# Kernel tuning notes

Hardware: AMD Instinct MI355X
Metric: run time of the kernel (lower is better)

Reference implementation:

```python
import jax, jax.numpy as jnp
import numpy as np

N_NODES = 100000
N_EDGES = 1600000


def _glorot(key, shape):
    lim = float(np.sqrt(6.0 / (shape[0] + shape[1])))
    return jax.random.uniform(key, shape, jnp.float32, -lim, lim)


def setup_inputs() -> dict:
    key = jax.random.key(0)
    ks = jax.random.split(key, 12)
    x = jax.random.normal(ks[0], (N_NODES, 8), jnp.float32)
    edge_index = jax.random.randint(ks[1], (2, N_EDGES), 0, N_NODES, jnp.int64)
    dims = [(8, 32), (32, 32), (32, 32), (32, 32), (32, 3)]
    params = {}
    for i, (din, dout) in enumerate(dims):
        params[f"W{i+1}"] = _glorot(ks[2 + i], (din, dout))
        params[f"b{i+1}"] = jnp.zeros((dout,), jnp.float32)
    return {"x": x, "edge_index": edge_index, **params}


def _gcn_norm(edge_index, num_nodes):
    # add self-loops, symmetric normalization (PyG GCNConv defaults)
    loops = jnp.arange(num_nodes, dtype=edge_index.dtype)
    row = jnp.concatenate([edge_index[0], loops])
    col = jnp.concatenate([edge_index[1], loops])
    deg = jax.ops.segment_sum(jnp.ones_like(col, jnp.float32), col,
                              num_segments=num_nodes)
    dinv = jnp.where(deg > 0, jax.lax.rsqrt(deg), 0.0)
    norm = dinv[row] * dinv[col]  # [E + N]
    return row, col, norm


def _gcn_conv(h, W, b, row, col, norm, num_nodes):
    h = h @ W                                   # [N, dout]
    msg = h[row] * norm[:, None]                # gather + scale
    out = jax.ops.segment_sum(msg, col, num_segments=num_nodes)
    return out + b


def reference(x, edge_index, W1, b1, W2, b2, W3, b3, W4, b4, W5, b5):
    row, col, norm = _gcn_norm(edge_index, N_NODES)
    lrelu = lambda h: jax.nn.leaky_relu(h, negative_slope=1.0)  # identity, kept faithful
    h = lrelu(_gcn_conv(x, W1, b1, row, col, norm, N_NODES))
    h = lrelu(_gcn_conv(h, W2, b2, row, col, norm, N_NODES))
    h = lrelu(_gcn_conv(h, W3, b3, row, col, norm, N_NODES))
    h = lrelu(_gcn_conv(h, W4, b4, row, col, norm, N_NODES))
    h = lrelu(_gcn_conv(h, W5, b5, row, col, norm, N_NODES))
    return h
```

## Files before the change

kernel.cpp:

```cpp
#include <hip/hip_runtime.h>
#include <hip/hip_bf16.h>

#define NN 100000
#define NE 1600000
#define NB 391
#define EPB 4096
#define NBLK 391
#define CAP 4608



__global__ __launch_bounds__(256) void prep_kernel(
    const unsigned int* __restrict__ ew, int* __restrict__ is64,
    const float* __restrict__ W1, const float* __restrict__ b1,
    const float* __restrict__ W2, const float* __restrict__ b2,
    const float* __restrict__ W3, const float* __restrict__ b3,
    const float* __restrict__ W4, const float* __restrict__ b4,
    const float* __restrict__ W5, const float* __restrict__ b5,
    float* __restrict__ Wt, float* __restrict__ cv,
    int* __restrict__ bcursor) {
    __shared__ int nz;
    __shared__ float w45[32 * 3], w345[32 * 3], w2345[32 * 3];
    int tid = threadIdx.x;
    if (tid == 0) nz = 0;
    __syncthreads();
    if (ew[2 * tid + 1] != 0) atomicAdd(&nz, 1);
    for (int i = tid; i < NB; i += 256) bcursor[i] = i * CAP;
    int i = tid / 3, j = tid - 3 * (tid / 3);
    if (tid < 96) {
        float s = 0.0f;
        for (int k = 0; k < 32; k++) s += W4[i * 32 + k] * W5[k * 3 + j];
        w45[i * 3 + j] = s;
    }
    __syncthreads();
    if (tid < 96) {
        float s = 0.0f;
        for (int k = 0; k < 32; k++) s += W3[i * 32 + k] * w45[k * 3 + j];
        w345[i * 3 + j] = s;
    }
    __syncthreads();
    if (tid < 96) {
        float s = 0.0f;
        for (int k = 0; k < 32; k++) s += W2[i * 32 + k] * w345[k * 3 + j];
        w2345[i * 3 + j] = s;
    }
    __syncthreads();
    if (tid < 32) {
        int ii = tid >> 2, jj = tid & 3;
        float s = 0.0f;
        if (jj < 3)
            for (int k = 0; k < 32; k++) s += W1[ii * 32 + k] * w2345[k * 3 + jj];
        Wt[tid] = s;
    }
    if (tid >= 32 && tid < 52) {
        int kk = (tid - 32) >> 2, jj = (tid - 32) & 3;
        float s = 0.0f;
        if (jj < 3) {
            if (kk == 0) for (int k = 0; k < 32; k++) s += b1[k] * w2345[k * 3 + jj];
            if (kk == 1) for (int k = 0; k < 32; k++) s += b2[k] * w345[k * 3 + jj];
            if (kk == 2) for (int k = 0; k < 32; k++) s += b3[k] * w45[k * 3 + jj];
            if (kk == 3) for (int k = 0; k < 32; k++) s += b4[k] * W5[k * 3 + jj];
            if (kk == 4) s = b5[jj];
        }
        cv[tid - 32] = s;
    }
    if (tid == 0) *is64 = (nz == 0) ? 1 : 0;
}


__global__ __launch_bounds__(512) void bucket_scatter_kernel(const void* __restrict__ ei,
                                                             const int* __restrict__ is64,
                                                             int* __restrict__ bcursor,
                                                             unsigned int* __restrict__ epacked,
                                                             int E) {
    __shared__ int lcount[NB];
    __shared__ int lstart[NB];
    __shared__ int lcur[NB];
    __shared__ int gbase[NB];
    __shared__ int ps[512];
    __shared__ unsigned int slotv[EPB];
    __shared__ unsigned short slotb[EPB];
    int tid = threadIdx.x;
    for (int i = tid; i < NB; i += 512) lcount[i] = 0;
    __syncthreads();
    int f = *is64;
    int base = blockIdx.x * EPB;
    int r[8], c[8];
    if (f == 0) {
        const int* e32 = (const int*)ei;
        const int4* e4 = (const int4*)ei;
#pragma unroll
        for (int k4 = 0; k4 < 2; k4++) {
            int e = base + (k4 * 512 + tid) * 4;
            if (e + 3 < E) {
                int4 v = e4[(base >> 2) + k4 * 512 + tid];
                r[4 * k4 + 0] = v.x; r[4 * k4 + 1] = v.y;
                r[4 * k4 + 2] = v.z; r[4 * k4 + 3] = v.w;
                int4 w = e4[((E + base) >> 2) + k4 * 512 + tid];
                c[4 * k4 + 0] = w.x; c[4 * k4 + 1] = w.y;
                c[4 * k4 + 2] = w.z; c[4 * k4 + 3] = w.w;
            } else {
#pragma unroll
                for (int j = 0; j < 4; j++) {
                    if (e + j < E) {
                        r[4 * k4 + j] = e32[e + j];
                        c[4 * k4 + j] = e32[E + e + j];
                    } else {
                        r[4 * k4 + j] = -1;
                    }
                }
            }
        }
    } else {
        const long long* e64 = (const long long*)ei;
#pragma unroll
        for (int k = 0; k < 8; k++) {
            int e = base + k * 512 + tid;
            if (e < E) {
                r[k] = (int)e64[e];
                c[k] = (int)e64[(long long)E + e];
            } else {
                r[k] = -1;
            }
        }
    }
#pragma unroll
    for (int k = 0; k < 8; k++)
        if (r[k] >= 0) atomicAdd(&lcount[c[k] >> 8], 1);
    __syncthreads();
    int v = (tid < NB) ? lcount[tid] : 0;
    int acc = v;
    ps[tid] = v;
    __syncthreads();
    for (int off = 1; off < 512; off <<= 1) {
        int y = (tid >= off) ? ps[tid - off] : 0;
        __syncthreads();
        acc += y;
        ps[tid] = acc;
        __syncthreads();
    }
    if (tid < NB) {
        int excl = acc - v;
        lstart[tid] = excl;
        lcur[tid] = excl;
    }
    __syncthreads();
#pragma unroll
    for (int k = 0; k < 8; k++) {
        if (r[k] >= 0) {
            int b = c[k] >> 8;
            int pos = atomicAdd(&lcur[b], 1);
            slotv[pos] = ((unsigned)(c[k] & 255) << 24) | (unsigned)r[k];
            slotb[pos] = (unsigned short)b;
        }
    }
    __syncthreads();
    for (int i = tid; i < NB; i += 512) {
        int cnt = lcount[i];
        gbase[i] = cnt ? atomicAdd(&bcursor[i], cnt) : 0;
    }
    __syncthreads();
    int rem = E - base;
    int total = (rem < EPB) ? rem : EPB;
    for (int s2 = tid; s2 < total; s2 += 512) {
        int b = slotb[s2];
        int dst = gbase[b] + (s2 - lstart[b]);
        if (dst < (b + 1) * CAP) epacked[dst] = slotv[s2];
    }
}


__global__ __launch_bounds__(512) void bucket_csr_kernel(const unsigned int* __restrict__ epacked,
                                                         const int* __restrict__ bcursor,
                                                         const float* __restrict__ x,
                                                         const float* __restrict__ Wt,
                                                         int* __restrict__ start,
                                                         int* __restrict__ degi,
                                                         float* __restrict__ dinv,
                                                         int* __restrict__ srow,
                                                         float4* __restrict__ Ta, int N) {
    __shared__ int lcount[256];
    __shared__ int lcur[256];
    __shared__ int ss[256];
    __shared__ float4 Wl[8];
    int b = blockIdx.x;
    int tid = threadIdx.x;
    if (tid < 8) Wl[tid] = ((const float4*)Wt)[tid];
    int s0 = b * CAP;
    int cnt = bcursor[b] - s0;
    if (cnt > CAP) cnt = CAP;
    if (tid < 256) lcount[tid] = 0;
    __syncthreads();
    for (int i = tid; i < cnt; i += 512) {
        unsigned int v = epacked[s0 + i];
        atomicAdd(&lcount[v >> 24], 1);
    }
    __syncthreads();
    int myc = 0, acc = 0;
    if (tid < 256) {
        myc = lcount[tid];
        acc = myc;
        ss[tid] = myc;
    }
    __syncthreads();
    for (int off = 1; off < 256; off <<= 1) {
        int y = 0;
        if (tid < 256 && tid >= off) y = ss[tid - off];
        __syncthreads();
        if (tid < 256) {
            acc += y;
            ss[tid] = acc;
        }
        __syncthreads();
    }
    if (tid < 256) {
        int excl = acc - myc;
        lcur[tid] = excl;
        int col = (b << 8) + tid;
        if (col < N) {
            start[col] = s0 + excl;
            degi[col] = myc;
            float d = 1.0f / sqrtf((float)myc + 1.0f);
            dinv[col] = d;
            const float4* x4 = (const float4*)x + col * 2;
            float4 av = x4[0], bv = x4[1];
            float xs[8] = {av.x, av.y, av.z, av.w, bv.x, bv.y, bv.z, bv.w};
            float4 o = make_float4(0.f, 0.f, 0.f, 0.f);
#pragma unroll
            for (int k = 0; k < 8; k++) {
                float4 w = Wl[k];
                o.x += xs[k] * w.x; o.y += xs[k] * w.y; o.z += xs[k] * w.z;
            }
            o.x *= d; o.y *= d; o.z *= d; o.w = 0.0f;
            Ta[col] = o;
        }
    }
    __syncthreads();
    for (int i = tid; i < cnt; i += 512) {
        unsigned int v = epacked[s0 + i];
        int p = atomicAdd(&lcur[v >> 24], 1);
        srow[s0 + p] = (int)(v & 0xFFFFFFu);
    }
}


template <bool LAST>
__global__ __launch_bounds__(256) void prop_kernel(
    const int* __restrict__ start, const int* __restrict__ degi,
    const int* __restrict__ srow, const float4* __restrict__ tin,
    const float* __restrict__ dinv, const float* __restrict__ cv, int k,
    float4* __restrict__ tout, float* __restrict__ out, int N) {
    int tid = blockIdx.x * 256 + threadIdx.x;
    int c = tid >> 3, q = tid & 7;
    if (c >= N) return;
    int s = start[c];
    int d = degi[c];
    float4 a = (q == 0) ? tin[c] : make_float4(0.f, 0.f, 0.f, 0.f);
    float4 a2 = make_float4(0.f, 0.f, 0.f, 0.f);
    int i = q;
    for (; i + 8 < d; i += 16) {
        int r0 = srow[s + i];
        int r1 = srow[s + i + 8];
        float4 v0 = tin[r0];
        float4 v1 = tin[r1];
        a.x += v0.x; a.y += v0.y; a.z += v0.z;
        a2.x += v1.x; a2.y += v1.y; a2.z += v1.z;
    }
    if (i < d) {
        float4 v = tin[srow[s + i]];
        a.x += v.x; a.y += v.y; a.z += v.z;
    }
    a.x += a2.x; a.y += a2.y; a.z += a2.z;
    a.x += __shfl_xor(a.x, 1); a.y += __shfl_xor(a.y, 1); a.z += __shfl_xor(a.z, 1);
    a.x += __shfl_xor(a.x, 2); a.y += __shfl_xor(a.y, 2); a.z += __shfl_xor(a.z, 2);
    a.x += __shfl_xor(a.x, 4); a.y += __shfl_xor(a.y, 4); a.z += __shfl_xor(a.z, 4);
    if (q == 0) {
        float dd = dinv[c];
        float cx = cv[k * 4 + 0], cy = cv[k * 4 + 1], cz = cv[k * 4 + 2];
        if (LAST) {
            out[c * 3 + 0] = dd * a.x + cx;
            out[c * 3 + 1] = dd * a.y + cy;
            out[c * 3 + 2] = dd * a.z + cz;
        } else {
            float d2 = dd * dd;
            float4 o;
            o.x = d2 * a.x + dd * cx;
            o.y = d2 * a.y + dd * cy;
            o.z = d2 * a.z + dd * cz;
            o.w = 0.0f;
            tout[c] = o;
        }
    }
}


extern "C" void kernel_launch(void* const* d_in, const int* in_sizes, int n_in,
                              void* d_out, int out_size, void* d_ws, size_t ws_size,
                              hipStream_t stream) {
    const float* x  = (const float*)d_in[0];
    const void*  ei = d_in[1];
    const float* W1 = (const float*)d_in[2];  const float* b1 = (const float*)d_in[3];
    const float* W2 = (const float*)d_in[4];  const float* b2 = (const float*)d_in[5];
    const float* W3 = (const float*)d_in[6];  const float* b3 = (const float*)d_in[7];
    const float* W4 = (const float*)d_in[8];  const float* b4 = (const float*)d_in[9];
    const float* W5 = (const float*)d_in[10]; const float* b5 = (const float*)d_in[11];
    float* out = (float*)d_out;

    char* p = (char*)d_ws;
    auto alloc = [&](size_t bytes) {
        char* r = p;
        p += (bytes + 255) & ~(size_t)255;
        return r;
    };
    int*   degi    = (int*)alloc(NN * 4);
    float* dinv    = (float*)alloc(NN * 4);
    int*   start   = (int*)alloc(NN * 4);
    int*   is64    = (int*)alloc(256);
    int*   bcursor = (int*)alloc(NB * 4);
    float* Wt      = (float*)alloc(8 * 4 * 4);
    float* cv      = (float*)alloc(5 * 4 * 4);
    unsigned int* epacked = (unsigned int*)alloc((size_t)NB * CAP * 4);
    int*          srow    = (int*)alloc((size_t)NB * CAP * 4);
    float4*       Ta      = (float4*)alloc((size_t)NN * 16);
    float4*       Tb      = (float4*)alloc((size_t)NN * 16);
    if ((size_t)(p - (char*)d_ws) > ws_size) return;

    int gP = (NN * 8 + 255) / 256;
    prep_kernel<<<1, 256, 0, stream>>>((const unsigned int*)ei, is64,
                                       W1, b1, W2, b2, W3, b3, W4, b4, W5, b5,
                                       Wt, cv, bcursor);
    bucket_scatter_kernel<<<NBLK, 512, 0, stream>>>(ei, is64, bcursor, epacked, NE);
    bucket_csr_kernel<<<NB, 512, 0, stream>>>(epacked, bcursor, x, Wt,
                                              start, degi, dinv, srow, Ta, NN);

    prop_kernel<false><<<gP, 256, 0, stream>>>(start, degi, srow, Ta, dinv, cv, 0, Tb, nullptr, NN);
    prop_kernel<false><<<gP, 256, 0, stream>>>(start, degi, srow, Tb, dinv, cv, 1, Ta, nullptr, NN);
    prop_kernel<false><<<gP, 256, 0, stream>>>(start, degi, srow, Ta, dinv, cv, 2, Tb, nullptr, NN);
    prop_kernel<false><<<gP, 256, 0, stream>>>(start, degi, srow, Tb, dinv, cv, 3, Ta, nullptr, NN);
    prop_kernel<true><<<gP, 256, 0, stream>>>(start, degi, srow, Ta, dinv, cv, 4, nullptr, out, NN);
}
```

Before: 173.0 us.

## Retune bucket scatter grid, use wave-shuffle scans, pack CSR metadata, narrow prop lanes

Splits edges across 512 scatter blocks of 3125 edges, dropping the vectorized int4 loads and the tail checks. Both prefix scans now use wavefront shuffle scans instead of LDS Hillis-Steele loops with many barriers. The CSR kernel stages the sorted rows in LDS so the srow writes are coalesced, and it packs start and degree into one int2 meta array. The prop kernels now use 4 lanes per node instead of 8 and recompute dinv from the degree instead of loading it. The goal is less global traffic, fewer barriers and better occupancy, at the cost of hardcoding NE and less parallelism per high-degree node.

```diff
diff --git a/kernel.cpp b/kernel.cpp
--- a/kernel.cpp
+++ b/kernel.cpp
@@ -4,8 +4,8 @@
 #define NN 100000
 #define NE 1600000
 #define NB 391
-#define EPB 4096
-#define NBLK 391
+#define EPB 3125
+#define NBLK 512
 #define CAP 4608
 
 
@@ -71,13 +71,12 @@
 __global__ __launch_bounds__(512) void bucket_scatter_kernel(const void* __restrict__ ei,
                                                              const int* __restrict__ is64,
                                                              int* __restrict__ bcursor,
-                                                             unsigned int* __restrict__ epacked,
-                                                             int E) {
+                                                             unsigned int* __restrict__ epacked) {
     __shared__ int lcount[NB];
     __shared__ int lstart[NB];
     __shared__ int lcur[NB];
     __shared__ int gbase[NB];
-    __shared__ int ps[512];
+    __shared__ int wsum[8];
     __shared__ unsigned int slotv[EPB];
     __shared__ unsigned short slotb[EPB];
     int tid = threadIdx.x;
@@ -85,68 +84,68 @@
     __syncthreads();
     int f = *is64;
     int base = blockIdx.x * EPB;
-    int r[8], c[8];
+    int r[7], c[7];
+    r[6] = -1;
     if (f == 0) {
         const int* e32 = (const int*)ei;
-        const int4* e4 = (const int4*)ei;
-#pragma unroll
-        for (int k4 = 0; k4 < 2; k4++) {
-            int e = base + (k4 * 512 + tid) * 4;
-            if (e + 3 < E) {
-                int4 v = e4[(base >> 2) + k4 * 512 + tid];
-                r[4 * k4 + 0] = v.x; r[4 * k4 + 1] = v.y;
-                r[4 * k4 + 2] = v.z; r[4 * k4 + 3] = v.w;
-                int4 w = e4[((E + base) >> 2) + k4 * 512 + tid];
-                c[4 * k4 + 0] = w.x; c[4 * k4 + 1] = w.y;
-                c[4 * k4 + 2] = w.z; c[4 * k4 + 3] = w.w;
-            } else {
-#pragma unroll
-                for (int j = 0; j < 4; j++) {
-                    if (e + j < E) {
-                        r[4 * k4 + j] = e32[e + j];
-                        c[4 * k4 + j] = e32[E + e + j];
-                    } else {
-                        r[4 * k4 + j] = -1;
-                    }
-                }
-            }
+#pragma unroll
+        for (int k = 0; k < 6; k++) {
+            int e = base + k * 512 + tid;
+            r[k] = e32[e];
+            c[k] = e32[NE + e];
+        }
+        if (tid < EPB - 6 * 512) {
+            int e = base + 6 * 512 + tid;
+            r[6] = e32[e];
+            c[6] = e32[NE + e];
         }
     } else {
         const long long* e64 = (const long long*)ei;
 #pragma unroll
-        for (int k = 0; k < 8; k++) {
+        for (int k = 0; k < 6; k++) {
             int e = base + k * 512 + tid;
-            if (e < E) {
-                r[k] = (int)e64[e];
-                c[k] = (int)e64[(long long)E + e];
-            } else {
-                r[k] = -1;
-            }
-        }
-    }
-#pragma unroll
-    for (int k = 0; k < 8; k++)
+            r[k] = (int)e64[e];
+            c[k] = (int)e64[(long long)NE + e];
+        }
+        if (tid < EPB - 6 * 512) {
+            int e = base + 6 * 512 + tid;
+            r[6] = (int)e64[e];
+            c[6] = (int)e64[(long long)NE + e];
+        }
+    }
+#pragma unroll
+    for (int k = 0; k < 7; k++)
         if (r[k] >= 0) atomicAdd(&lcount[c[k] >> 8], 1);
     __syncthreads();
+    int lane = tid & 63, w = tid >> 6;
     int v = (tid < NB) ? lcount[tid] : 0;
     int acc = v;
-    ps[tid] = v;
-    __syncthreads();
-    for (int off = 1; off < 512; off <<= 1) {
-        int y = (tid >= off) ? ps[tid - off] : 0;
-        __syncthreads();
-        acc += y;
-        ps[tid] = acc;
-        __syncthreads();
-    }
+#pragma unroll
+    for (int off = 1; off < 64; off <<= 1) {
+        int y = __shfl_up(acc, off);
+        if (lane >= off) acc += y;
+    }
+    if (lane == 63) wsum[w] = acc;
+    __syncthreads();
+    if (tid == 0) {
+        int s = 0;
+#pragma unroll
+        for (int j = 0; j < 8; j++) { int t = wsum[j]; wsum[j] = s; s += t; }
+    }
+    __syncthreads();
+    acc += wsum[w];
     if (tid < NB) {
         int excl = acc - v;
         lstart[tid] = excl;
         lcur[tid] = excl;
     }
-    __syncthreads();
-#pragma unroll
-    for (int k = 0; k < 8; k++) {
+    for (int i = tid; i < NB; i += 512) {
+        int cnt = lcount[i];
+        gbase[i] = cnt ? atomicAdd(&bcursor[i], cnt) : 0;
+    }
+    __syncthreads();
+#pragma unroll
+    for (int k = 0; k < 7; k++) {
         if (r[k] >= 0) {
             int b = c[k] >> 8;
             int pos = atomicAdd(&lcur[b], 1);
@@ -155,14 +154,7 @@
         }
     }
     __syncthreads();
-    for (int i = tid; i < NB; i += 512) {
-        int cnt = lcount[i];
-        gbase[i] = cnt ? atomicAdd(&bcursor[i], cnt) : 0;
-    }
-    __syncthreads();
-    int rem = E - base;
-    int total = (rem < EPB) ? rem : EPB;
-    for (int s2 = tid; s2 < total; s2 += 512) {
+    for (int s2 = tid; s2 < EPB; s2 += 512) {
         int b = slotb[s2];
         int dst = gbase[b] + (s2 - lstart[b]);
         if (dst < (b + 1) * CAP) epacked[dst] = slotv[s2];
@@ -174,15 +166,14 @@
                                                          const int* __restrict__ bcursor,
                                                          const float* __restrict__ x,
                                                          const float* __restrict__ Wt,
-                                                         int* __restrict__ start,
-                                                         int* __restrict__ degi,
-                                                         float* __restrict__ dinv,
+                                                         int2* __restrict__ meta,
                                                          int* __restrict__ srow,
                                                          float4* __restrict__ Ta, int N) {
     __shared__ int lcount[256];
     __shared__ int lcur[256];
-    __shared__ int ss[256];
+    __shared__ int wsum[4];
     __shared__ float4 Wl[8];
+    __shared__ int sbuf[CAP];
     int b = blockIdx.x;
     int tid = threadIdx.x;
     if (tid < 8) Wl[tid] = ((const float4*)Wt)[tid];
@@ -196,40 +187,37 @@
         atomicAdd(&lcount[v >> 24], 1);
     }
     __syncthreads();
-    int myc = 0, acc = 0;
+    int lane = tid & 63, w = tid >> 6;
+    int myc = (tid < 256) ? lcount[tid] : 0;
+    int acc = myc;
+#pragma unroll
+    for (int off = 1; off < 64; off <<= 1) {
+        int y = __shfl_up(acc, off);
+        if (lane >= off) acc += y;
+    }
+    if (lane == 63 && w < 4) wsum[w] = acc;
+    __syncthreads();
+    if (tid == 0) {
+        int s = 0;
+#pragma unroll
+        for (int j = 0; j < 4; j++) { int t = wsum[j]; wsum[j] = s; s += t; }
+    }
+    __syncthreads();
     if (tid < 256) {
-        myc = lcount[tid];
-        acc = myc;
-        ss[tid] = myc;
-    }
-    __syncthreads();
-    for (int off = 1; off < 256; off <<= 1) {
-        int y = 0;
-        if (tid < 256 && tid >= off) y = ss[tid - off];
-        __syncthreads();
-        if (tid < 256) {
-            acc += y;
-            ss[tid] = acc;
-        }
-        __syncthreads();
-    }
-    if (tid < 256) {
-        int excl = acc - myc;
+        int excl = acc - myc + wsum[w];
         lcur[tid] = excl;
         int col = (b << 8) + tid;
         if (col < N) {
-            start[col] = s0 + excl;
-            degi[col] = myc;
+            meta[col] = make_int2(s0 + excl, myc);
             float d = 1.0f / sqrtf((float)myc + 1.0f);
-            dinv[col] = d;
             const float4* x4 = (const float4*)x + col * 2;
             float4 av = x4[0], bv = x4[1];
             float xs[8] = {av.x, av.y, av.z, av.w, bv.x, bv.y, bv.z, bv.w};
             float4 o = make_float4(0.f, 0.f, 0.f, 0.f);
 #pragma unroll
             for (int k = 0; k < 8; k++) {
-                float4 w = Wl[k];
-                o.x += xs[k] * w.x; o.y += xs[k] * w.y; o.z += xs[k] * w.z;
+                float4 ww = Wl[k];
+                o.x += xs[k] * ww.x; o.y += xs[k] * ww.y; o.z += xs[k] * ww.z;
             }
             o.x *= d; o.y *= d; o.z *= d; o.w = 0.0f;
             Ta[col] = o;
@@ -239,28 +227,30 @@
     for (int i = tid; i < cnt; i += 512) {
         unsigned int v = epacked[s0 + i];
         int p = atomicAdd(&lcur[v >> 24], 1);
-        srow[s0 + p] = (int)(v & 0xFFFFFFu);
-    }
+        sbuf[p] = (int)(v & 0xFFFFFFu);
+    }
+    __syncthreads();
+    for (int i = tid; i < cnt; i += 512) srow[s0 + i] = sbuf[i];
 }
 
 
 template <bool LAST>
 __global__ __launch_bounds__(256) void prop_kernel(
-    const int* __restrict__ start, const int* __restrict__ degi,
-    const int* __restrict__ srow, const float4* __restrict__ tin,
-    const float* __restrict__ dinv, const float* __restrict__ cv, int k,
+    const int2* __restrict__ meta, const int* __restrict__ srow,
+    const float4* __restrict__ tin, const float* __restrict__ cv, int k,
     float4* __restrict__ tout, float* __restrict__ out, int N) {
     int tid = blockIdx.x * 256 + threadIdx.x;
-    int c = tid >> 3, q = tid & 7;
+    int c = tid >> 2, q = tid & 3;
     if (c >= N) return;
-    int s = start[c];
-    int d = degi[c];
+    int2 m = meta[c];
+    int s = m.x;
+    int d = m.y;
     float4 a = (q == 0) ? tin[c] : make_float4(0.f, 0.f, 0.f, 0.f);
     float4 a2 = make_float4(0.f, 0.f, 0.f, 0.f);
     int i = q;
-    for (; i + 8 < d; i += 16) {
+    for (; i + 4 < d; i += 8) {
         int r0 = srow[s + i];
-        int r1 = srow[s + i + 8];
+        int r1 = srow[s + i + 4];
         float4 v0 = tin[r0];
         float4 v1 = tin[r1];
         a.x += v0.x; a.y += v0.y; a.z += v0.z;
@@ -273,9 +263,8 @@
     a.x += a2.x; a.y += a2.y; a.z += a2.z;
     a.x += __shfl_xor(a.x, 1); a.y += __shfl_xor(a.y, 1); a.z += __shfl_xor(a.z, 1);
     a.x += __shfl_xor(a.x, 2); a.y += __shfl_xor(a.y, 2); a.z += __shfl_xor(a.z, 2);
-    a.x += __shfl_xor(a.x, 4); a.y += __shfl_xor(a.y, 4); a.z += __shfl_xor(a.z, 4);
     if (q == 0) {
-        float dd = dinv[c];
+        float dd = 1.0f / sqrtf((float)d + 1.0f);
         float cx = cv[k * 4 + 0], cy = cv[k * 4 + 1], cz = cv[k * 4 + 2];
         if (LAST) {
             out[c * 3 + 0] = dd * a.x + cx;
@@ -312,9 +301,7 @@
         p += (bytes + 255) & ~(size_t)255;
         return r;
     };
-    int*   degi    = (int*)alloc(NN * 4);
-    float* dinv    = (float*)alloc(NN * 4);
-    int*   start   = (int*)alloc(NN * 4);
+    int2*  meta    = (int2*)alloc((size_t)NN * 8);
     int*   is64    = (int*)alloc(256);
     int*   bcursor = (int*)alloc(NB * 4);
     float* Wt      = (float*)alloc(8 * 4 * 4);
@@ -325,17 +312,17 @@
     float4*       Tb      = (float4*)alloc((size_t)NN * 16);
     if ((size_t)(p - (char*)d_ws) > ws_size) return;
 
-    int gP = (NN * 8 + 255) / 256;
+    int gP = (NN * 4 + 255) / 256;
     prep_kernel<<<1, 256, 0, stream>>>((const unsigned int*)ei, is64,
                                        W1, b1, W2, b2, W3, b3, W4, b4, W5, b5,
                                        Wt, cv, bcursor);
-    bucket_scatter_kernel<<<NBLK, 512, 0, stream>>>(ei, is64, bcursor, epacked, NE);
+    bucket_scatter_kernel<<<NBLK, 512, 0, stream>>>(ei, is64, bcursor, epacked);
     bucket_csr_kernel<<<NB, 512, 0, stream>>>(epacked, bcursor, x, Wt,
-                                              start, degi, dinv, srow, Ta, NN);
-
-    prop_kernel<false><<<gP, 256, 0, stream>>>(start, degi, srow, Ta, dinv, cv, 0, Tb, nullptr, NN);
-    prop_kernel<false><<<gP, 256, 0, stream>>>(start, degi, srow, Tb, dinv, cv, 1, Ta, nullptr, NN);
-    prop_kernel<false><<<gP, 256, 0, stream>>>(start, degi, srow, Ta, dinv, cv, 2, Tb, nullptr, NN);
-    prop_kernel<false><<<gP, 256, 0, stream>>>(start, degi, srow, Tb, dinv, cv, 3, Ta, nullptr, NN);
-    prop_kernel<true><<<gP, 256, 0, stream>>>(start, degi, srow, Ta, dinv, cv, 4, nullptr, out, NN);
-}
+                                              meta, srow, Ta, NN);
+
+    prop_kernel<false><<<gP, 256, 0, stream>>>(meta, srow, Ta, cv, 0, Tb, nullptr, NN);
+    prop_kernel<false><<<gP, 256, 0, stream>>>(meta, srow, Tb, cv, 1, Ta, nullptr, NN);
+    prop_kernel<false><<<gP, 256, 0, stream>>>(meta, srow, Ta, cv, 2, Tb, nullptr, NN);
+    prop_kernel<false><<<gP, 256, 0, stream>>>(meta, srow, Tb, cv, 3, Ta, nullptr, NN);
+    prop_kernel<true><<<gP, 256, 0, stream>>>(meta, srow, Ta, cv, 4, nullptr, out, NN);
+}
```

Result: faster. 168.9 us (-2.4%).
